# Kernel tuning notes

Measured on AMD Instinct MI355X. Metric: run time of the kernel, lower is better.

Reference implementation:

```python
import jax, jax.numpy as jnp
import numpy as np

K_OUTLIER = 16   # decomposition_topk default k
Q = 127.0        # int8 symmetric quant scale


def _quantize(mat):
    # per-row abs-max symmetric quantization; torch .to(int8) truncates toward
    # zero, which matches XLA's float->int convert semantics.
    mmax = jnp.max(jnp.abs(mat), axis=-1)                      # [...,]
    q = (mat * (Q / mmax)[..., None]).astype(jnp.int8)
    return q, mmax


def setup_inputs() -> dict:
    key = jax.random.key(0)
    k1, k2, k3 = jax.random.split(key, 3)
    B, I, O = 4096, 2048, 2048
    x = jax.random.normal(k1, (B, I), jnp.float32)
    weight = jax.random.normal(k2, (O, I), jnp.float32) * 0.02  # nn.Linear convention [out, in]
    bias = jax.random.normal(k3, (O,), jnp.float32) * 0.02
    return {"x": x, "weight": weight, "bias": bias}


def reference(x, weight, bias):
    # --- weight-side prep (done once in __init__ in the torch module) ---
    col_max = jnp.max(jnp.abs(weight), axis=0)                 # [I] abs-max per input column
    idx = jax.lax.top_k(col_max, K_OUTLIER)[1]                 # [k] outlier input columns
    w_unq = weight[:, idx].T                                   # [k, O] fp outlier weights
    w0 = weight.at[:, idx].set(0.0)                            # zero outlier columns
    w_q, w_max = _quantize(w0)                                 # int8 [O, I], fp [O]

    # --- activation side ---
    x_unq = x[:, idx]                                          # [B, k]
    x1 = x.at[:, idx].set(0.0)
    x_q, x_max = _quantize(x1)                                 # int8 [B, I], fp [B]

    # int8 matmul accumulated in int32 (MatMulInteger), then dequantize
    res_q_i32 = jnp.matmul(x_q.astype(jnp.int32), w_q.T.astype(jnp.int32))  # [B, O]
    mx = x_max[:, None] * w_max[None, :]                       # outer product of row/col maxes
    res_q = (res_q_i32.astype(jnp.float32) / (Q * Q)).astype(jnp.float16).astype(jnp.float32) * mx

    # fp outlier path + bias
    res_unq = x_unq @ w_unq + bias                             # [B, O]
    return res_q + res_unq
```

## Files before the change

### kernel.cpp

```cpp
#include <hip/hip_runtime.h>
#include <hip/hip_fp16.h>
#include <stdint.h>

#define I_DIM 2048
#define O_DIM 2048
#define B_DIM 4096
#define KOUT 16

typedef int i32x4 __attribute__((ext_vector_type(4)));
typedef float f32x4 __attribute__((ext_vector_type(4)));
typedef _Float16 f16x8 __attribute__((ext_vector_type(8)));

#define TO_LDS(p) ((__attribute__((address_space(3))) void*)(p))
#define TO_GLB(p) ((const __attribute__((address_space(1))) void*)(p))

__global__ void colmax_kernel(const float* __restrict__ W, unsigned* __restrict__ cm) {
  int j = blockIdx.x * 256 + threadIdx.x;
  int i0 = blockIdx.y * 64;
  float m = 0.0f;
  const float* p = W + (size_t)i0 * I_DIM + j;
  for (int i = 0; i < 64; ++i)
    m = fmaxf(m, fabsf(p[(size_t)i * I_DIM]));
  atomicMax(cm + j, __float_as_uint(m));
}

__global__ void topk_kernel(const unsigned* __restrict__ cm, int* __restrict__ idx,
                            float* __restrict__ keep) {
  int t = threadIdx.x;
  const float4* c4 = (const float4*)cm;
  float4 a = c4[t * 2], b = c4[t * 2 + 1];
  float v[8] = {a.x, a.y, a.z, a.w, b.x, b.y, b.z, b.w};
  for (int j = t; j < I_DIM; j += 256) keep[j] = 1.0f;
  __shared__ float wm_[4];
  __shared__ int wi_[4];
  __shared__ int sel;
  for (int k = 0; k < KOUT; ++k) {
    float m = v[0]; int mi = 0;
#pragma unroll
    for (int r = 1; r < 8; ++r) if (v[r] > m) { m = v[r]; mi = r; }
    int gi = t * 8 + mi;
#pragma unroll
    for (int s = 32; s; s >>= 1) {
      float om = __shfl_down(m, s);
      int oi = __shfl_down(gi, s);
      if (om > m) { m = om; gi = oi; }
    }
    if ((t & 63) == 0) { wm_[t >> 6] = m; wi_[t >> 6] = gi; }
    __syncthreads();
    if (t == 0) {
      float bm = wm_[0]; int bi = wi_[0];
      for (int w2 = 1; w2 < 4; ++w2) if (wm_[w2] > bm) { bm = wm_[w2]; bi = wi_[w2]; }
      idx[k] = bi; keep[bi] = 0.0f; sel = bi;
    }
    __syncthreads();
    if (t == (sel >> 3)) v[sel & 7] = -1.0f;
  }
}

__global__ __launch_bounds__(256) void quant_kernel(
    const float* __restrict__ X, const float* __restrict__ W,
    const float* __restrict__ keep, const int* __restrict__ idx,
    signed char* __restrict__ xq, signed char* __restrict__ wq,
    float* __restrict__ xmax, float* __restrict__ wmax,
    _Float16* __restrict__ xunqh,
    _Float16* __restrict__ wunqh) {
  int b = blockIdx.x;
  int t = threadIdx.x;
  bool isW = b < O_DIM;
  int r = isW ? b : (b - O_DIM);
  const float* src = isW ? (W + (size_t)r * I_DIM) : (X + (size_t)r * I_DIM);
  const float4* s4 = (const float4*)src;
  const float4* k4 = (const float4*)keep;
  float4 v0 = s4[t], v1 = s4[t + 256];
  float4 k0 = k4[t], k1 = k4[t + 256];
  v0.x *= k0.x; v0.y *= k0.y; v0.z *= k0.z; v0.w *= k0.w;
  v1.x *= k1.x; v1.y *= k1.y; v1.z *= k1.z; v1.w *= k1.w;
  float m = fmaxf(fmaxf(fmaxf(fabsf(v0.x), fabsf(v0.y)), fmaxf(fabsf(v0.z), fabsf(v0.w))),
                  fmaxf(fmaxf(fabsf(v1.x), fabsf(v1.y)), fmaxf(fabsf(v1.z), fabsf(v1.w))));
#pragma unroll
  for (int s = 32; s; s >>= 1) m = fmaxf(m, __shfl_xor(m, s));
  __shared__ float red[4];
  if ((t & 63) == 0) red[t >> 6] = m;
  __syncthreads();
  m = fmaxf(fmaxf(red[0], red[1]), fmaxf(red[2], red[3]));
  float sc = 127.0f / m;
  unsigned p0 = (unsigned char)(signed char)(int)(v0.x * sc)
              | ((unsigned)(unsigned char)(signed char)(int)(v0.y * sc) << 8)
              | ((unsigned)(unsigned char)(signed char)(int)(v0.z * sc) << 16)
              | ((unsigned)(unsigned char)(signed char)(int)(v0.w * sc) << 24);
  unsigned p1 = (unsigned char)(signed char)(int)(v1.x * sc)
              | ((unsigned)(unsigned char)(signed char)(int)(v1.y * sc) << 8)
              | ((unsigned)(unsigned char)(signed char)(int)(v1.z * sc) << 16)
              | ((unsigned)(unsigned char)(signed char)(int)(v1.w * sc) << 24);
  unsigned* qout = (unsigned*)(isW ? (wq + (size_t)r * I_DIM) : (xq + (size_t)r * I_DIM));
  qout[t] = p0;
  qout[t + 256] = p1;
  if (t == 0) { if (isW) wmax[r] = m; else xmax[r] = m; }
  if (t < KOUT) {
    float ov = src[idx[t]];
    _Float16* u = isW ? (wunqh + (size_t)r * 32) : (xunqh + (size_t)r * 32);
    u[t] = (_Float16)ov;
    u[t + KOUT] = (_Float16)0.0f;
  }
}

__global__ __launch_bounds__(256) void gemm_kernel(
    const signed char* __restrict__ Aq,
    const signed char* __restrict__ Bq,
    const float* __restrict__ xmaxg,
    const float* __restrict__ wmaxg,
    const _Float16* __restrict__ xunqh,
    const _Float16* __restrict__ wunqh,
    const float* __restrict__ biasg,
    float* __restrict__ out) {
  constexpr int N = O_DIM, K = I_DIM;
  __shared__ __align__(16) signed char smem[16384];
  signed char* As = smem;
  signed char* Bs = smem + 8192;

  const int tid = threadIdx.x;
  const int lane = tid & 63;
  const int wave = tid >> 6;
  const int wm = (wave & 1) * 64;
  const int wn = (wave >> 1) * 64;
  const int m0 = blockIdx.y * 128;
  const int n0 = blockIdx.x * 128;
  const int row0 = tid >> 2;
  const int col0 = ((((tid & 3) - (row0 >> 1)) & 3) * 16);
  const int fm = lane & 15;
  const int q = lane >> 4;

  i32x4 acc[4][4] = {};

  for (int kt = 0; kt < K; kt += 64) {
    const signed char* ga0 = Aq + (size_t)(m0 + row0) * K + kt + col0;
    const signed char* gb0 = Bq + (size_t)(n0 + row0) * K + kt + col0;
    __builtin_amdgcn_global_load_lds(TO_GLB(ga0), TO_LDS(As + wave * 1024), 16, 0, 0);
    __builtin_amdgcn_global_load_lds(TO_GLB(ga0 + (size_t)64 * K), TO_LDS(As + 4096 + wave * 1024), 16, 0, 0);
    __builtin_amdgcn_global_load_lds(TO_GLB(gb0), TO_LDS(Bs + wave * 1024), 16, 0, 0);
    __builtin_amdgcn_global_load_lds(TO_GLB(gb0 + (size_t)64 * K), TO_LDS(Bs + 4096 + wave * 1024), 16, 0, 0);
    __syncthreads();
    i32x4 af[4], bf[4];
#pragma unroll
    for (int i = 0; i < 4; ++i) {
      int r = wm + i * 16 + fm;
      af[i] = *(const i32x4*)(As + r * 64 + (((q + (r >> 1)) & 3) << 4));
    }
#pragma unroll
    for (int i = 0; i < 4; ++i) {
      int r = wn + i * 16 + fm;
      bf[i] = *(const i32x4*)(Bs + r * 64 + (((q + (r >> 1)) & 3) << 4));
    }
#pragma unroll
    for (int i = 0; i < 4; ++i)
#pragma unroll
      for (int j = 0; j < 4; ++j)
        acc[i][j] = __builtin_amdgcn_mfma_i32_16x16x64_i8(af[i], bf[j], acc[i][j], 0, 0, 0);
    __syncthreads();
  }

  f16x8 afh[4], bfh[4];
#pragma unroll
  for (int i = 0; i < 4; ++i)
    afh[i] = *(const f16x8*)(xunqh + (size_t)(m0 + wm + i * 16 + fm) * 32 + q * 8);
#pragma unroll
  for (int j = 0; j < 4; ++j)
    bfh[j] = *(const f16x8*)(wunqh + (size_t)(n0 + wn + j * 16 + fm) * 32 + q * 8);

#pragma unroll
  for (int i = 0; i < 4; ++i) {
    f32x4 xmv = *(const f32x4*)(xmaxg + m0 + wm + i * 16 + q * 4);
#pragma unroll
    for (int j = 0; j < 4; ++j) {
      int cl = n0 + wn + j * 16 + fm;
      float wmv = wmaxg[cl];
      float bv = biasg[cl];
      f32x4 c;
#pragma unroll
      for (int r = 0; r < 4; ++r) {
        float v = (float)acc[i][j][r] / 16129.0f;
        v = __half2float(__float2half(v));
        c[r] = v * (xmv[r] * wmv) + bv;
      }
      c = __builtin_amdgcn_mfma_f32_16x16x32_f16(afh[i], bfh[j], c, 0, 0, 0);
#pragma unroll
      for (int r = 0; r < 4; ++r)
        out[(size_t)(m0 + wm + i * 16 + q * 4 + r) * N + cl] = c[r];
    }
  }
}

extern "C" void kernel_launch(void* const* d_in, const int* in_sizes, int n_in,
                              void* d_out, int out_size, void* d_ws, size_t ws_size,
                              hipStream_t stream) {
  const float* x    = (const float*)d_in[0];
  const float* w    = (const float*)d_in[1];
  const float* bias = (const float*)d_in[2];
  float* out = (float*)d_out;
  char* ws = (char*)d_ws;

  unsigned* cm     = (unsigned*)(ws + 0);
  int* idx         = (int*)(ws + 8192);
  float* keep      = (float*)(ws + 8320);
  float* w_max     = (float*)(ws + 16512);
  float* x_max     = (float*)(ws + 24704);
  _Float16* x_unqh = (_Float16*)(ws + 41088);
  _Float16* w_unqh = (_Float16*)(ws + 303232);
  signed char* w_q = (signed char*)(ws + 434304);
  signed char* x_q = (signed char*)(ws + 4628608);

  hipMemsetAsync(cm, 0, 8192, stream);
  colmax_kernel<<<dim3(8, 32), 256, 0, stream>>>(w, cm);
  topk_kernel<<<1, 256, 0, stream>>>(cm, idx, keep);
  quant_kernel<<<O_DIM + B_DIM, 256, 0, stream>>>(x, w, keep, idx, x_q, w_q,
                                                  x_max, w_max, x_unqh, w_unqh);
  gemm_kernel<<<dim3(O_DIM / 128, B_DIM / 128), 256, 0, stream>>>(
      x_q, w_q, x_max, w_max, x_unqh, w_unqh, bias, out);
}
```

Baseline: 149.9 us.

## Double-buffer GEMM K-tiles with BK=128 and XCD-aware block swizzle

The int8 GEMM loop now uses two 32KB LDS buffers and prefetches the next 128-wide K tile while running MFMAs on the current one. This replaces the single-buffered 64-wide tile that waited on every load. Blocks are also remapped so each XCD covers a contiguous 8x8 region of output tiles, which should improve L2 reuse. LDS grows to 64KB per block and launch_bounds asks for 2 blocks per CU, so occupancy and register pressure may be affected.

```diff
diff --git a/kernel.cpp b/kernel.cpp
--- a/kernel.cpp
+++ b/kernel.cpp
@@ -104,7 +104,7 @@
   }
 }
 
-__global__ __launch_bounds__(256) void gemm_kernel(
+__global__ __launch_bounds__(256, 2) void gemm_kernel(
     const signed char* __restrict__ Aq,
     const signed char* __restrict__ Bq,
     const float* __restrict__ xmaxg,
@@ -114,48 +114,69 @@
     const float* __restrict__ biasg,
     float* __restrict__ out) {
   constexpr int N = O_DIM, K = I_DIM;
-  __shared__ __align__(16) signed char smem[16384];
-  signed char* As = smem;
-  signed char* Bs = smem + 8192;
+  __shared__ __align__(16) signed char smem[2][32768];
 
   const int tid = threadIdx.x;
   const int lane = tid & 63;
   const int wave = tid >> 6;
   const int wm = (wave & 1) * 64;
   const int wn = (wave >> 1) * 64;
-  const int m0 = blockIdx.y * 128;
-  const int n0 = blockIdx.x * 128;
-  const int row0 = tid >> 2;
-  const int col0 = ((((tid & 3) - (row0 >> 1)) & 3) * 16);
+
+  const int lid = blockIdx.y * gridDim.x + blockIdx.x;
+  const int xcd = lid & 7;
+  const int pos = lid >> 3;
+  const int by = (xcd >> 1) * 8 + (pos >> 3);
+  const int bx = (xcd & 1) * 8 + (pos & 7);
+  const int m0 = by * 128;
+  const int n0 = bx * 128;
+
+  const int srow = tid >> 3;
+  const int cslot = tid & 7;
   const int fm = lane & 15;
   const int q = lane >> 4;
 
   i32x4 acc[4][4] = {};
 
-  for (int kt = 0; kt < K; kt += 64) {
-    const signed char* ga0 = Aq + (size_t)(m0 + row0) * K + kt + col0;
-    const signed char* gb0 = Bq + (size_t)(n0 + row0) * K + kt + col0;
-    __builtin_amdgcn_global_load_lds(TO_GLB(ga0), TO_LDS(As + wave * 1024), 16, 0, 0);
-    __builtin_amdgcn_global_load_lds(TO_GLB(ga0 + (size_t)64 * K), TO_LDS(As + 4096 + wave * 1024), 16, 0, 0);
-    __builtin_amdgcn_global_load_lds(TO_GLB(gb0), TO_LDS(Bs + wave * 1024), 16, 0, 0);
-    __builtin_amdgcn_global_load_lds(TO_GLB(gb0 + (size_t)64 * K), TO_LDS(Bs + 4096 + wave * 1024), 16, 0, 0);
-    __syncthreads();
-    i32x4 af[4], bf[4];
-#pragma unroll
-    for (int i = 0; i < 4; ++i) {
-      int r = wm + i * 16 + fm;
-      af[i] = *(const i32x4*)(As + r * 64 + (((q + (r >> 1)) & 3) << 4));
-    }
-#pragma unroll
-    for (int i = 0; i < 4; ++i) {
-      int r = wn + i * 16 + fm;
-      bf[i] = *(const i32x4*)(Bs + r * 64 + (((q + (r >> 1)) & 3) << 4));
-    }
-#pragma unroll
-    for (int i = 0; i < 4; ++i)
-#pragma unroll
-      for (int j = 0; j < 4; ++j)
-        acc[i][j] = __builtin_amdgcn_mfma_i32_16x16x64_i8(af[i], bf[j], acc[i][j], 0, 0, 0);
+  auto stage = [&](int buf, int kt) {
+    signed char* As = &smem[buf][0];
+    signed char* Bs = &smem[buf][16384];
+#pragma unroll
+    for (int a = 0; a < 4; ++a) {
+      const int row = a * 32 + srow;
+      const int gch = (cslot - (row >> 1)) & 7;
+      const signed char* ga = Aq + (size_t)(m0 + row) * K + kt + gch * 16;
+      const signed char* gb = Bq + (size_t)(n0 + row) * K + kt + gch * 16;
+      __builtin_amdgcn_global_load_lds(TO_GLB(ga), TO_LDS(As + a * 4096 + tid * 16), 16, 0, 0);
+      __builtin_amdgcn_global_load_lds(TO_GLB(gb), TO_LDS(Bs + a * 4096 + tid * 16), 16, 0, 0);
+    }
+  };
+
+  stage(0, 0);
+  __syncthreads();
+
+#pragma unroll 2
+  for (int t = 0; t < K / 128; ++t) {
+    const int cur = t & 1;
+    if (t < K / 128 - 1) stage(cur ^ 1, (t + 1) * 128);
+    const signed char* As = &smem[cur][0];
+    const signed char* Bs = &smem[cur][16384];
+#pragma unroll
+    for (int s = 0; s < 2; ++s) {
+      i32x4 af[4], bf[4];
+      const int q8 = s * 4 + q;
+#pragma unroll
+      for (int i = 0; i < 4; ++i) {
+        const int ra = wm + i * 16 + fm;
+        af[i] = *(const i32x4*)(As + ra * 128 + (((q8 + (ra >> 1)) & 7) << 4));
+        const int rb = wn + i * 16 + fm;
+        bf[i] = *(const i32x4*)(Bs + rb * 128 + (((q8 + (rb >> 1)) & 7) << 4));
+      }
+#pragma unroll
+      for (int i = 0; i < 4; ++i)
+#pragma unroll
+        for (int j = 0; j < 4; ++j)
+          acc[i][j] = __builtin_amdgcn_mfma_i32_16x16x64_i8(af[i], bf[j], acc[i][j], 0, 0, 0);
+    }
     __syncthreads();
   }
 
```

Measured after the change: 144.9 us. 3.4% less time.
